# Kernel optimization log

Measured on AMD Instinct MI355X. Metric: run time of the kernel, lower is better.

Reference implementation:

```python
import jax, jax.numpy as jnp
import numpy as np

B, N, D = 16, 2048, 64

def setup_inputs() -> dict:
    key = jax.random.key(0)
    kq, kk, kv = jax.random.split(key, 3)
    queries = jax.random.normal(kq, (B, N, D), dtype=jnp.float32)
    keys = jax.random.normal(kk, (B, N, D), dtype=jnp.float32)
    values = jax.random.normal(kv, (B, N, D), dtype=jnp.float32)
    scaling_factor = jnp.asarray(np.sqrt(D), dtype=jnp.float32)
    return {"queries": queries, "keys": keys, "values": values, "scaling_factor": scaling_factor}

def reference(queries, keys, values, scaling_factor):
    # scores: [B, N, N] = Q K^T / scale
    scores = jnp.einsum('bqd,bkd->bqk', queries, keys) / scaling_factor
    atn = jax.nn.softmax(scores, axis=2)
    return jnp.einsum('bqk,bkd->bqd', atn, values)
```

## Files before the change

### kernel.cpp

```cpp
#include <hip/hip_runtime.h>
#include <hip/hip_bf16.h>

#define BATCH 16
#define SEQ 2048
#define DIM 64

typedef __attribute__((ext_vector_type(8))) __bf16 bf16x8;
typedef __attribute__((ext_vector_type(8))) unsigned short u16x8;
typedef __attribute__((ext_vector_type(2))) unsigned int u32x2;
typedef __attribute__((ext_vector_type(4))) unsigned int u32x4;
typedef __attribute__((ext_vector_type(16))) float f32x16;

#if __has_builtin(__builtin_amdgcn_exp2f)
#define EXP2F(x) __builtin_amdgcn_exp2f(x)
#else
#define EXP2F(x) __expf(0.69314718055994531f * (x))
#endif

__device__ __forceinline__ unsigned short f2bf_hw(float f) {
    __bf16 h = (__bf16)f;
    return __builtin_bit_cast(unsigned short, h);
}

__device__ __forceinline__ unsigned int pk_bf16(float lo, float hi) {
    unsigned int a = f2bf_hw(lo), b = f2bf_hw(hi);
    return a | (b << 16);
}

__device__ __forceinline__ bf16x8 ld_bf8_g(const unsigned short* p) {
    u16x8 u = *(const u16x8*)p;
    return __builtin_bit_cast(bf16x8, u);
}

__device__ __forceinline__ void half_swap(unsigned int a, unsigned int b,
                                          unsigned int& lo, unsigned int& hi) {
#if __has_builtin(__builtin_amdgcn_permlane32_swap)
    u32x2 r = __builtin_amdgcn_permlane32_swap(a, b, false, false);
    lo = r[0];
    hi = r[1];
#else
    unsigned int sa = (unsigned int)__shfl_xor((int)a, 32);
    unsigned int sb = (unsigned int)__shfl_xor((int)b, 32);
    const bool hh = (threadIdx.x & 32) != 0;
    lo = hh ? sb : a;
    hi = hh ? b : sa;
#endif
}

__global__ __launch_bounds__(256)
void preconvert_kv(const float* __restrict__ K, const float* __restrict__ V,
                   unsigned short* __restrict__ Ks, unsigned short* __restrict__ Vts) {
    __shared__ float vt[128 * 65];
    const int tid = threadIdx.x;
    if (blockIdx.x < 256) {
        const int b = blockIdx.x >> 4;
        const int t = blockIdx.x & 15;
        const float* src = K + ((size_t)(b * SEQ + t * 128)) * DIM;
        unsigned short* dst = Ks + ((size_t)(b * 16 + t)) * 8192;
        #pragma unroll
        for (int p = 0; p < 4; ++p) {
            const int cid = p * 256 + tid;
            const int key = cid >> 3, g = cid & 7;
            const int d0 = (g >> 1) * 16 + (g & 1) * 8;
            float4 x0 = *(const float4*)(src + key * DIM + d0);
            float4 x1 = *(const float4*)(src + key * DIM + d0 + 4);
            u16x8 o;
            o[0] = f2bf_hw(x0.x); o[1] = f2bf_hw(x0.y); o[2] = f2bf_hw(x0.z); o[3] = f2bf_hw(x0.w);
            o[4] = f2bf_hw(x1.x); o[5] = f2bf_hw(x1.y); o[6] = f2bf_hw(x1.z); o[7] = f2bf_hw(x1.w);
            *(u16x8*)(dst + (g * 128 + key) * 8) = o;
        }
    } else {
        const int vb = blockIdx.x - 256;
        const int b = vb >> 4;
        const int t = vb & 15;
        const float* src = V + ((size_t)(b * SEQ + t * 128)) * DIM;
        #pragma unroll
        for (int p = 0; p < 8; ++p) {
            const int f = p * 256 + tid;
            const int row = f >> 4, c4 = (f & 15) << 2;
            float4 x = *(const float4*)(src + row * DIM + c4);
            vt[row * 65 + c4 + 0] = x.x; vt[row * 65 + c4 + 1] = x.y;
            vt[row * 65 + c4 + 2] = x.z; vt[row * 65 + c4 + 3] = x.w;
        }
        __syncthreads();
        unsigned short* dst = Vts + ((size_t)(b * 16 + t)) * 8192;
        #pragma unroll
        for (int p = 0; p < 4; ++p) {
            const int cid = p * 256 + tid;
            const int g = cid >> 6, d = cid & 63;
            const int k0 = (g >> 1) * 16 + (g & 1) * 8;
            u16x8 o;
            #pragma unroll
            for (int j = 0; j < 8; ++j) o[j] = f2bf_hw(vt[(k0 + j) * 65 + d]);
            *(u16x8*)(dst + (g * 64 + d) * 8) = o;
        }
    }
}

__global__ __launch_bounds__(256, 2)
void attn_flash_kernel(const float* __restrict__ Q,
                       const unsigned short* __restrict__ Ks,
                       const unsigned short* __restrict__ Vts,
                       const float* __restrict__ scaling,
                       float* __restrict__ O) {
    __shared__ float comb[3 * 64 * 66];

    const int tid  = threadIdx.x;
    const int w    = tid >> 6;
    const int lane = tid & 63;
    const int m    = lane & 31;
    const int h    = lane >> 5;

    const int x  = blockIdx.x;
    const int b  = ((x & 7) << 1) | ((x >> 3) & 1);
    const int q0 = (x >> 4) * 64;

    const float csc = 1.4426950408889634f / scaling[0];

    bf16x8 aq0[4], aq1[4];
    #pragma unroll
    for (int s = 0; s < 2; ++s) {
        const float* qsrc = Q + ((size_t)(b * SEQ + q0 + s * 32 + m)) * DIM + h * 8;
        #pragma unroll
        for (int c = 0; c < 4; ++c) {
            float4 x0 = *(const float4*)(qsrc + c * 16);
            float4 x1 = *(const float4*)(qsrc + c * 16 + 4);
            u32x4 pk;
            pk[0] = pk_bf16(x0.x * csc, x0.y * csc);
            pk[1] = pk_bf16(x0.z * csc, x0.w * csc);
            pk[2] = pk_bf16(x1.x * csc, x1.y * csc);
            pk[3] = pk_bf16(x1.z * csc, x1.w * csc);
            (s ? aq1 : aq0)[c] = __builtin_bit_cast(bf16x8, pk);
        }
    }

    f32x16 Oacc0[2], Oacc1[2];
    #pragma unroll
    for (int dt = 0; dt < 2; ++dt)
        #pragma unroll
        for (int r = 0; r < 16; ++r) { Oacc0[dt][r] = 0.f; Oacc1[dt][r] = 0.f; }
    float psum0 = 0.f, psum1 = 0.f;

    const unsigned short* Kbase = Ks + ((size_t)(b * 16 + w * 4)) * 8192;
    const unsigned short* Vbase = Vts + ((size_t)(b * 16 + w * 4)) * 8192;

    bf16x8 kc[4];
    #pragma unroll
    for (int c = 0; c < 4; ++c)
        kc[c] = ld_bf8_g(&Kbase[((c * 2 + h) * 128 + m) * 8]);
    bf16x8 bv[2][2];
    #pragma unroll
    for (int c2 = 0; c2 < 2; ++c2)
        #pragma unroll
        for (int dt = 0; dt < 2; ++dt)
            bv[c2][dt] = ld_bf8_g(&Vbase[((c2 * 2 + h) * 64 + dt * 32 + m) * 8]);

    #pragma unroll 1
    for (int st = 0; st < 16; ++st) {
        f32x16 S0, S1;
        #pragma unroll
        for (int r = 0; r < 16; ++r) { S0[r] = 0.f; S1[r] = 0.f; }
        __builtin_amdgcn_s_setprio(1);
        #pragma unroll
        for (int c = 0; c < 4; ++c) {
            S0 = __builtin_amdgcn_mfma_f32_32x32x16_bf16(kc[c], aq0[c], S0, 0, 0, 0);
            S1 = __builtin_amdgcn_mfma_f32_32x32x16_bf16(kc[c], aq1[c], S1, 0, 0, 0);
        }
        __builtin_amdgcn_s_setprio(0);

        const int stn = (st < 15) ? st + 1 : 15;
        const unsigned short* Ktn = Kbase + (size_t)(stn >> 2) * 8192;
        const int tn = stn & 3;
        bf16x8 kn[4];
        #pragma unroll
        for (int c = 0; c < 4; ++c)
            kn[c] = ld_bf8_g(&Ktn[((c * 2 + h) * 128 + tn * 32 + m) * 8]);

        unsigned int d0a[8], d0b[8];
        #pragma unroll
        for (int k = 0; k < 4; ++k) {
            float a0 = EXP2F(S0[4 * k + 0]), a1 = EXP2F(S0[4 * k + 1]);
            float a2 = EXP2F(S0[4 * k + 2]), a3 = EXP2F(S0[4 * k + 3]);
            psum0 += (a0 + a1) + (a2 + a3);
            d0a[2 * k + 0] = pk_bf16(a0, a1);
            d0a[2 * k + 1] = pk_bf16(a2, a3);
            float b0 = EXP2F(S1[4 * k + 0]), b1 = EXP2F(S1[4 * k + 1]);
            float b2 = EXP2F(S1[4 * k + 2]), b3 = EXP2F(S1[4 * k + 3]);
            psum1 += (b0 + b1) + (b2 + b3);
            d0b[2 * k + 0] = pk_bf16(b0, b1);
            d0b[2 * k + 1] = pk_bf16(b2, b3);
        }

        bf16x8 pb0[2], pb1[2];
        #pragma unroll
        for (int c2 = 0; c2 < 2; ++c2) {
            u32x4 bw0, bw1;
            unsigned int lo, hi;
            half_swap(d0a[4 * c2 + 0], d0a[4 * c2 + 2], lo, hi);
            bw0[0] = lo; bw0[2] = hi;
            half_swap(d0a[4 * c2 + 1], d0a[4 * c2 + 3], lo, hi);
            bw0[1] = lo; bw0[3] = hi;
            half_swap(d0b[4 * c2 + 0], d0b[4 * c2 + 2], lo, hi);
            bw1[0] = lo; bw1[2] = hi;
            half_swap(d0b[4 * c2 + 1], d0b[4 * c2 + 3], lo, hi);
            bw1[1] = lo; bw1[3] = hi;
            pb0[c2] = __builtin_bit_cast(bf16x8, bw0);
            pb1[c2] = __builtin_bit_cast(bf16x8, bw1);
        }

        __builtin_amdgcn_s_setprio(1);
        #pragma unroll
        for (int c2 = 0; c2 < 2; ++c2)
            #pragma unroll
            for (int dt = 0; dt < 2; ++dt) {
                Oacc0[dt] = __builtin_amdgcn_mfma_f32_32x32x16_bf16(bv[c2][dt], pb0[c2], Oacc0[dt], 0, 0, 0);
                Oacc1[dt] = __builtin_amdgcn_mfma_f32_32x32x16_bf16(bv[c2][dt], pb1[c2], Oacc1[dt], 0, 0, 0);
            }
        __builtin_amdgcn_s_setprio(0);

        const unsigned short* Vtn = Vbase + (size_t)(stn >> 2) * 8192;
        #pragma unroll
        for (int c2 = 0; c2 < 2; ++c2)
            #pragma unroll
            for (int dt = 0; dt < 2; ++dt)
                bv[c2][dt] = ld_bf8_g(&Vtn[(((2 * tn + c2) * 2 + h) * 64 + dt * 32 + m) * 8]);

        #pragma unroll
        for (int c = 0; c < 4; ++c) kc[c] = kn[c];
    }

    float l0 = psum0 + __shfl_xor(psum0, 32);
    float l1 = psum1 + __shfl_xor(psum1, 32);
    if (w > 0) {
        float* dst = comb + ((w - 1) * 64 + lane) * 66;
        #pragma unroll
        for (int dt = 0; dt < 2; ++dt)
            #pragma unroll
            for (int r = 0; r < 16; ++r) {
                dst[dt * 16 + r]      = Oacc0[dt][r];
                dst[33 + dt * 16 + r] = Oacc1[dt][r];
            }
        dst[32] = l0;
        dst[65] = l1;
    }
    __syncthreads();
    if (w == 0) {
        const float* p0 = comb + (0 * 64 + lane) * 66;
        const float* p1 = comb + (1 * 64 + lane) * 66;
        const float* p2 = comb + (2 * 64 + lane) * 66;
        const float invl0 = 1.0f / (l0 + p0[32] + p1[32] + p2[32]);
        const float invl1 = 1.0f / (l1 + p0[65] + p1[65] + p2[65]);
        float* orow0 = O + ((size_t)(b * SEQ + q0 + m)) * DIM;
        float* orow1 = O + ((size_t)(b * SEQ + q0 + 32 + m)) * DIM;
        #pragma unroll
        for (int dt = 0; dt < 2; ++dt) {
            #pragma unroll
            for (int k = 0; k < 4; ++k) {
                float4 o4;
                #pragma unroll
                for (int j = 0; j < 4; ++j) {
                    const int r = 4 * k + j;
                    ((float*)&o4)[j] = (Oacc0[dt][r] + p0[dt * 16 + r] + p1[dt * 16 + r]
                                        + p2[dt * 16 + r]) * invl0;
                }
                *(float4*)(orow0 + dt * 32 + 8 * k + 4 * h) = o4;
                #pragma unroll
                for (int j = 0; j < 4; ++j) {
                    const int r = 4 * k + j;
                    ((float*)&o4)[j] = (Oacc1[dt][r] + p0[33 + dt * 16 + r] + p1[33 + dt * 16 + r]
                                        + p2[33 + dt * 16 + r]) * invl1;
                }
                *(float4*)(orow1 + dt * 32 + 8 * k + 4 * h) = o4;
            }
        }
    }
}

extern "C" void kernel_launch(void* const* d_in, const int* in_sizes, int n_in,
                              void* d_out, int out_size, void* d_ws, size_t ws_size,
                              hipStream_t stream) {
    const float* Q = (const float*)d_in[0];
    const float* K = (const float*)d_in[1];
    const float* V = (const float*)d_in[2];
    const float* scaling = (const float*)d_in[3];
    float* O = (float*)d_out;

    unsigned short* Ks  = (unsigned short*)d_ws;
    unsigned short* Vts = Ks + (size_t)BATCH * 16 * 8192;

    preconvert_kv<<<dim3(512), dim3(256), 0, stream>>>(K, V, Ks, Vts);
    attn_flash_kernel<<<dim3(BATCH * (SEQ / 64)), dim3(256), 0, stream>>>(Q, Ks, Vts, scaling, O);
}
```

Baseline: 101.1 us.

## Software-pipeline QK^T of next tile with softmax/PV of current tile

Restructures the main loop into a two-stage ping-pong pipeline. The S = K·Q MFMAs for the next key tile are issued before the exp/pack and P·V MFMAs of the current tile, with K prefetched two tiles ahead. This lets matrix-core work overlap with the transcendental and VALU softmax work and hides more load latency. In exchange it holds extra accumulator and K registers, which may raise register pressure and lower occupancy. It also issues one redundant S computation at the end.

```diff
diff --git a/kernel.cpp b/kernel.cpp
--- a/kernel.cpp
+++ b/kernel.cpp
@@ -144,53 +144,50 @@
     const unsigned short* Kbase = Ks + ((size_t)(b * 16 + w * 4)) * 8192;
     const unsigned short* Vbase = Vts + ((size_t)(b * 16 + w * 4)) * 8192;
 
-    bf16x8 kc[4];
-    #pragma unroll
-    for (int c = 0; c < 4; ++c)
-        kc[c] = ld_bf8_g(&Kbase[((c * 2 + h) * 128 + m) * 8]);
+    bf16x8 kcA[4], kcB[4];
     bf16x8 bv[2][2];
-    #pragma unroll
-    for (int c2 = 0; c2 < 2; ++c2)
-        #pragma unroll
-        for (int dt = 0; dt < 2; ++dt)
-            bv[c2][dt] = ld_bf8_g(&Vbase[((c2 * 2 + h) * 64 + dt * 32 + m) * 8]);
-
-    #pragma unroll 1
-    for (int st = 0; st < 16; ++st) {
-        f32x16 S0, S1;
-        #pragma unroll
-        for (int r = 0; r < 16; ++r) { S0[r] = 0.f; S1[r] = 0.f; }
-        __builtin_amdgcn_s_setprio(1);
+    f32x16 SA0, SA1, SB0, SB1;
+
+    auto load_k = [&](bf16x8* dst, int s) {
+        const unsigned short* Kt = Kbase + (size_t)(s >> 2) * 8192;
+        const int t = s & 3;
+        #pragma unroll
+        for (int c = 0; c < 4; ++c)
+            dst[c] = ld_bf8_g(&Kt[((c * 2 + h) * 128 + t * 32 + m) * 8]);
+    };
+    auto load_v = [&](int s) {
+        const unsigned short* Vt = Vbase + (size_t)(s >> 2) * 8192;
+        const int t = s & 3;
+        #pragma unroll
+        for (int c2 = 0; c2 < 2; ++c2)
+            #pragma unroll
+            for (int dt = 0; dt < 2; ++dt)
+                bv[c2][dt] = ld_bf8_g(&Vt[(((2 * t + c2) * 2 + h) * 64 + dt * 32 + m) * 8]);
+    };
+    auto calc_s = [&](f32x16& s0, f32x16& s1, const bf16x8* kc) {
+        #pragma unroll
+        for (int r = 0; r < 16; ++r) { s0[r] = 0.f; s1[r] = 0.f; }
         #pragma unroll
         for (int c = 0; c < 4; ++c) {
-            S0 = __builtin_amdgcn_mfma_f32_32x32x16_bf16(kc[c], aq0[c], S0, 0, 0, 0);
-            S1 = __builtin_amdgcn_mfma_f32_32x32x16_bf16(kc[c], aq1[c], S1, 0, 0, 0);
-        }
-        __builtin_amdgcn_s_setprio(0);
-
-        const int stn = (st < 15) ? st + 1 : 15;
-        const unsigned short* Ktn = Kbase + (size_t)(stn >> 2) * 8192;
-        const int tn = stn & 3;
-        bf16x8 kn[4];
-        #pragma unroll
-        for (int c = 0; c < 4; ++c)
-            kn[c] = ld_bf8_g(&Ktn[((c * 2 + h) * 128 + tn * 32 + m) * 8]);
-
+            s0 = __builtin_amdgcn_mfma_f32_32x32x16_bf16(kc[c], aq0[c], s0, 0, 0, 0);
+            s1 = __builtin_amdgcn_mfma_f32_32x32x16_bf16(kc[c], aq1[c], s1, 0, 0, 0);
+        }
+    };
+    auto softmax_pv = [&](const f32x16& Sv0, const f32x16& Sv1) {
         unsigned int d0a[8], d0b[8];
         #pragma unroll
         for (int k = 0; k < 4; ++k) {
-            float a0 = EXP2F(S0[4 * k + 0]), a1 = EXP2F(S0[4 * k + 1]);
-            float a2 = EXP2F(S0[4 * k + 2]), a3 = EXP2F(S0[4 * k + 3]);
+            float a0 = EXP2F(Sv0[4 * k + 0]), a1 = EXP2F(Sv0[4 * k + 1]);
+            float a2 = EXP2F(Sv0[4 * k + 2]), a3 = EXP2F(Sv0[4 * k + 3]);
             psum0 += (a0 + a1) + (a2 + a3);
             d0a[2 * k + 0] = pk_bf16(a0, a1);
             d0a[2 * k + 1] = pk_bf16(a2, a3);
-            float b0 = EXP2F(S1[4 * k + 0]), b1 = EXP2F(S1[4 * k + 1]);
-            float b2 = EXP2F(S1[4 * k + 2]), b3 = EXP2F(S1[4 * k + 3]);
+            float b0 = EXP2F(Sv1[4 * k + 0]), b1 = EXP2F(Sv1[4 * k + 1]);
+            float b2 = EXP2F(Sv1[4 * k + 2]), b3 = EXP2F(Sv1[4 * k + 3]);
             psum1 += (b0 + b1) + (b2 + b3);
             d0b[2 * k + 0] = pk_bf16(b0, b1);
             d0b[2 * k + 1] = pk_bf16(b2, b3);
         }
-
         bf16x8 pb0[2], pb1[2];
         #pragma unroll
         for (int c2 = 0; c2 < 2; ++c2) {
@@ -207,7 +204,6 @@
             pb0[c2] = __builtin_bit_cast(bf16x8, bw0);
             pb1[c2] = __builtin_bit_cast(bf16x8, bw1);
         }
-
         __builtin_amdgcn_s_setprio(1);
         #pragma unroll
         for (int c2 = 0; c2 < 2; ++c2)
@@ -217,16 +213,31 @@
                 Oacc1[dt] = __builtin_amdgcn_mfma_f32_32x32x16_bf16(bv[c2][dt], pb1[c2], Oacc1[dt], 0, 0, 0);
             }
         __builtin_amdgcn_s_setprio(0);
-
-        const unsigned short* Vtn = Vbase + (size_t)(stn >> 2) * 8192;
-        #pragma unroll
-        for (int c2 = 0; c2 < 2; ++c2)
-            #pragma unroll
-            for (int dt = 0; dt < 2; ++dt)
-                bv[c2][dt] = ld_bf8_g(&Vtn[(((2 * tn + c2) * 2 + h) * 64 + dt * 32 + m) * 8]);
-
-        #pragma unroll
-        for (int c = 0; c < 4; ++c) kc[c] = kn[c];
+    };
+
+    load_k(kcA, 0);
+    load_k(kcB, 1);
+    load_v(0);
+    calc_s(SA0, SA1, kcA);
+
+    #pragma unroll 1
+    for (int it = 0; it < 8; ++it) {
+        const int e = 2 * it;
+        {
+            const int s2 = (e + 2 < 16) ? e + 2 : 15;
+            load_k(kcA, s2);
+            calc_s(SB0, SB1, kcB);
+            softmax_pv(SA0, SA1);
+            load_v(e + 1);
+        }
+        {
+            const int s3 = (e + 3 < 16) ? e + 3 : 15;
+            load_k(kcB, s3);
+            calc_s(SA0, SA1, kcA);
+            softmax_pv(SB0, SB1);
+            const int s2 = (e + 2 < 16) ? e + 2 : 15;
+            load_v(s2);
+        }
     }
 
     float l0 = psum0 + __shfl_xor(psum0, 32);
```

New measurement: 103.5 us. 1.02x slower.
